# Kernel tuning notes

Hardware: AMD Instinct MI355X
Metric: run time of the kernel (lower is better)

## Reference

```python
import jax, jax.numpy as jnp
import numpy as np

B, S, D = 2, 2048, 1024
H, DK, DV = 16, 64, 64
MASKED = True


def setup_inputs() -> dict:
    key = jax.random.key(0)
    ks = jax.random.split(key, 12)
    s = 0.02
    inp = {
        "Q": jax.random.normal(ks[0], (B, S, D), jnp.float32),
        "K": jax.random.normal(ks[1], (B, S, D), jnp.float32),
        "V": jax.random.normal(ks[2], (B, S, D), jnp.float32),
        "pad_mask": jax.random.randint(ks[3], (B, S), 0, 2, jnp.int32),
        "Wq": jax.random.normal(ks[4], (D, H * DK), jnp.float32) * s,
        "bq": jnp.zeros((H * DK,), jnp.float32),
        "Wk": jax.random.normal(ks[5], (D, H * DK), jnp.float32) * s,
        "bk": jnp.zeros((H * DK,), jnp.float32),
        "Wv": jax.random.normal(ks[6], (D, H * DV), jnp.float32) * s,
        "bv": jnp.zeros((H * DV,), jnp.float32),
        "Wo": jax.random.normal(ks[7], (H * DV, D), jnp.float32) * s,
        "bo": jnp.zeros((D,), jnp.float32),
    }
    return inp


def _split(x):
    # [B,S,H*d] -> [B,H,S,d]
    b, s, _ = x.shape
    return x.reshape(b, s, H, -1).transpose(0, 2, 1, 3)


def reference(Q, K, V, pad_mask, Wq, bq, Wk, bk, Wv, bv, Wo, bo):
    q = _split(Q @ Wq + bq)  # [B,H,S,DK]
    k = _split(K @ Wk + bk)  # [B,H,S,DK]
    v = _split(V @ Wv + bv)  # [B,H,S,DV]

    scores = jnp.einsum("bhqd,bhkd->bhqk", q, k) / np.sqrt(DK)
    mask = pad_mask[:, None, None, :].astype(jnp.float32)  # [B,1,1,S]
    if MASKED:
        causal = jnp.triu(jnp.ones((S, S), jnp.float32), k=1)[None, None]
        mask = ((mask + causal) > 0).astype(jnp.float32)
    scores = scores - 1e9 * mask

    attn = jax.nn.softmax(scores, axis=-1)
    out = jnp.einsum("bhqk,bhkd->bhqd", attn, v)  # [B,H,S,DV]
    out = out.transpose(0, 2, 1, 3).reshape(B, S, H * DV)
    return out @ Wo + bo
```

## Files before the change

### kernel.cpp

```cpp
#include <hip/hip_runtime.h>

typedef unsigned short u16;
typedef unsigned int u32;

typedef __attribute__((ext_vector_type(8))) short bfrag;
typedef __attribute__((ext_vector_type(4))) float f32x4;
typedef __attribute__((ext_vector_type(8))) u16 u16x8;
typedef __attribute__((ext_vector_type(4))) u16 u16x4;

constexpr int S = 2048;
constexpr int HN = 16;
constexpr float QSCALE = 0.18033688011112042f;
constexpr float NBIG   = -1.442695e9f;

__device__ __forceinline__ u16 f2b(float f) {
  u32 u = __builtin_bit_cast(u32, f);
  return (u16)((u + 0x7FFFu + ((u >> 16) & 1u)) >> 16);
}
__device__ __forceinline__ float b2f(u16 v) {
  u32 u = (u32)v << 16;
  return __builtin_bit_cast(float, u);
}
__device__ __forceinline__ u32 cvtpk(float lo, float hi) {
  u32 d;
  asm("v_cvt_pk_bf16_f32 %0, %1, %2" : "=v"(d) : "v"(lo), "v"(hi));
  return d;
}
__device__ __forceinline__ float fexp2(float x) { return __builtin_amdgcn_exp2f(x); }

__device__ __forceinline__ f32x4 mfma16(bfrag a, bfrag b, f32x4 c) {
  return __builtin_amdgcn_mfma_f32_16x16x32_bf16(a, b, c, 0, 0, 0);
}

__device__ __forceinline__ void gload_lds16(const void* g, void* l) {
  __builtin_amdgcn_global_load_lds(
      (const __attribute__((address_space(1))) u32*)g,
      (__attribute__((address_space(3))) u32*)l, 16, 0, 0);
}

__global__ __launch_bounds__(256) void wtrans_kernel(
    const float* __restrict__ W0, const float* __restrict__ W1,
    const float* __restrict__ W2, const float* __restrict__ W3,
    u16* __restrict__ ws)
{
  const float* W = blockIdx.z == 0 ? W0 : blockIdx.z == 1 ? W1 : blockIdx.z == 2 ? W2 : W3;
  const float sc = blockIdx.z == 0 ? QSCALE : 1.0f;
  u16* WT = ws + (size_t)blockIdx.z * (1u << 20);
  __shared__ u16 tile[64 * 65];
  const int t = threadIdx.x;
  const int k0 = blockIdx.y * 64, n0 = blockIdx.x * 64;
#pragma unroll
  for (int i = 0; i < 4; ++i) {
    int idx = i * 256 + t;
    int r = idx >> 4, c4 = (idx & 15) * 4;
    float4 v = *(const float4*)&W[(size_t)(k0 + r) * 1024 + n0 + c4];
    tile[r * 65 + c4 + 0] = f2b(v.x * sc);
    tile[r * 65 + c4 + 1] = f2b(v.y * sc);
    tile[r * 65 + c4 + 2] = f2b(v.z * sc);
    tile[r * 65 + c4 + 3] = f2b(v.w * sc);
  }
  __syncthreads();
#pragma unroll
  for (int i = 0; i < 2; ++i) {
    int idx = i * 256 + t;
    int n = idx >> 3, k8 = (idx & 7) * 8;
    u16x8 o;
#pragma unroll
    for (int j = 0; j < 8; ++j) o[j] = tile[(k8 + j) * 65 + n];
    *(u16x8*)&WT[(size_t)(n0 + n) * 1024 + k0 + k8] = o;
  }
}

__global__ __launch_bounds__(256) void cvt_kernel(
    const float* __restrict__ A0, const float* __restrict__ A1,
    const float* __restrict__ A2, u16* __restrict__ outbase)
{
  const float* A = blockIdx.y == 0 ? A0 : blockIdx.y == 1 ? A1 : A2;
  u16* dst = outbase + (size_t)blockIdx.y * (4u << 20);
  size_t i = ((size_t)blockIdx.x * 256 + threadIdx.x) * 8;
  float4 v0 = *(const float4*)&A[i];
  float4 v1 = *(const float4*)&A[i + 4];
  union { u32 w[4]; u16x8 v; } o;
  o.w[0] = cvtpk(v0.x, v0.y); o.w[1] = cvtpk(v0.z, v0.w);
  o.w[2] = cvtpk(v1.x, v1.y); o.w[3] = cvtpk(v1.z, v1.w);
  *(u16x8*)&dst[i] = o.v;
}

__global__ __launch_bounds__(256) void pscan_kernel(
    const int* __restrict__ pad, u16* __restrict__ idxc, u16* __restrict__ posT,
    int* __restrict__ eqt, float* __restrict__ colsumg)
{
  __shared__ int wtot[4];
  __shared__ int cntS;
  const int b = blockIdx.x;
  const int t = threadIdx.x, lane = t & 63, w = t >> 6;
  for (int i = t; i < 1024; i += 256) colsumg[b * 1024 + i] = 0.f;
  int4 p0 = *(const int4*)&pad[b * 2048 + t * 8];
  int4 p1 = *(const int4*)&pad[b * 2048 + t * 8 + 4];
  int u[8] = {p0.x == 0, p0.y == 0, p0.z == 0, p0.w == 0,
              p1.x == 0, p1.y == 0, p1.z == 0, p1.w == 0};
  int ps[8], run = 0;
#pragma unroll
  for (int j = 0; j < 8; ++j) { run += u[j]; ps[j] = run; }
  int sc = run;
#pragma unroll
  for (int o = 1; o < 64; o <<= 1) {
    int v = __shfl_up(sc, o);
    if (lane >= o) sc += v;
  }
  if (lane == 63) wtot[w] = sc;
  __syncthreads();
  int base = 0;
#pragma unroll
  for (int i = 0; i < 4; ++i) if (i < w) base += wtot[i];
  int excl = base + sc - run;
#pragma unroll
  for (int j = 0; j < 8; ++j)
    if (u[j]) idxc[b * 2048 + excl + ps[j] - 1] = (u16)(t * 8 + j);
  if ((t & 7) == 7) eqt[b * 32 + (t >> 3)] = base + sc;
  if (t == 255) cntS = base + sc;
  __syncthreads();
  const int cnt = cntS;
#pragma unroll
  for (int j = 0; j < 8; ++j) {
    int e = t * 8 + j;
    int pv = u[j] ? (excl + ps[j] - 1) : (cnt + e - excl - ps[j]);
    posT[b * 2048 + e] = (u16)pv;
  }
  for (int j = cnt + t; j < 2048; j += 256) idxc[b * 2048 + j] = 0x7FFF;
}

__global__ __launch_bounds__(256) void vgather_kernel(
    const u16* __restrict__ vb, const u16* __restrict__ idxc, u16* __restrict__ vTc)
{
  __shared__ u16 tile[64 * 65];
  const int ti = blockIdx.x, bh = blockIdx.y, b = bh >> 4;
  const int t = threadIdx.x;
#pragma unroll
  for (int i = 0; i < 2; ++i) {
    int idx = i * 256 + t;
    int r = idx >> 3, c8 = (idx & 7) * 8;
    int o = idxc[b * 2048 + ti * 64 + r];
    u16x8 in = {};
    if (o != 0x7FFF) in = *(const u16x8*)&vb[((size_t)bh * 2048 + o) * 64 + c8];
#pragma unroll
    for (int j = 0; j < 8; ++j) tile[r * 65 + c8 + j] = in[j];
  }
  __syncthreads();
#pragma unroll
  for (int i = 0; i < 2; ++i) {
    int idx = i * 256 + t;
    int dv = idx >> 3, s8 = (idx & 7) * 8;
    u16x8 o_;
#pragma unroll
    for (int j = 0; j < 8; ++j) o_[j] = tile[(s8 + j) * 65 + dv];
    int a = s8 >> 5, bb = (s8 >> 4) & 1, cc = (s8 >> 3) & 1;
    int s0l = a * 32 + cc * 16 + bb * 4;
    int x = (dv & 7) << 3;
    u16x4 lo = {o_[0], o_[1], o_[2], o_[3]};
    u16x4 hi = {o_[4], o_[5], o_[6], o_[7]};
    size_t rowbase = ((size_t)bh * 64 + dv) * S + ti * 64;
    *(u16x4*)&vTc[rowbase + (s0l ^ x)] = lo;
    *(u16x4*)&vTc[rowbase + ((s0l + 8) ^ x)] = hi;
  }
}

template <int CMODE>
__device__ __forceinline__ void gemm_core(
    u16* As, u16* Bs,
    const u16* __restrict__ A, const u16* __restrict__ Bt,
    const float* __restrict__ bias, void* __restrict__ Cout,
    int N, int K, int bn, int bm, float bscale,
    const u16* __restrict__ posT, float* __restrict__ csum)
{
  const int tid = threadIdx.x;
  const int wid = tid >> 6, lane = tid & 63;
  const int g = lane >> 4, c = lane & 15;
  const int wr = wid >> 1, wc = wid & 1;

  f32x4 acc[4][2] = {};

  const int nkt = K >> 6;
  for (int kt = 0; kt < nkt; ++kt) {
#pragma unroll
    for (int p = 0; p < 4; ++p) {
      int off = (p * 4 + wid) * 1024 + (lane << 4);
      int row = off >> 7, colb = off & 127;
      gload_lds16(&A[(size_t)(bm * 128 + row) * K + kt * 64 +
                     ((colb ^ ((row & 7) << 4)) >> 1)],
                  (char*)As + (p * 4 + wid) * 1024);
    }
#pragma unroll
    for (int p = 0; p < 2; ++p) {
      int off = (p * 4 + wid) * 1024 + (lane << 4);
      int row = off >> 7, colb = off & 127;
      gload_lds16(&Bt[(size_t)(bn * 64 + row) * K + kt * 64 +
                      ((colb ^ ((row & 7) << 4)) >> 1)],
                  (char*)Bs + (p * 4 + wid) * 1024);
    }
    __syncthreads();

#pragma unroll
    for (int ks = 0; ks < 2; ++ks) {
      bfrag af[4], bf[2];
#pragma unroll
      for (int mi = 0; mi < 4; ++mi) {
        int row = wr * 64 + mi * 16 + c;
        af[mi] = *(const bfrag*)&As[row * 64 + ((ks * 32 + g * 8) ^ ((row & 7) << 3))];
      }
#pragma unroll
      for (int ni = 0; ni < 2; ++ni) {
        int row = wc * 32 + ni * 16 + c;
        bf[ni] = *(const bfrag*)&Bs[row * 64 + ((ks * 32 + g * 8) ^ ((row & 7) << 3))];
      }
#pragma unroll
      for (int mi = 0; mi < 4; ++mi)
#pragma unroll
        for (int ni = 0; ni < 2; ++ni)
          acc[mi][ni] = mfma16(af[mi], bf[ni], acc[mi][ni]);
    }
    __syncthreads();
  }

  float colacc[2] = {0.f, 0.f};
#pragma unroll
  for (int mi = 0; mi < 4; ++mi) {
#pragma unroll
    for (int ni = 0; ni < 2; ++ni) {
#pragma unroll
      for (int j = 0; j < 4; ++j) {
        int rowg = bm * 128 + wr * 64 + mi * 16 + g * 4 + j;
        int colg = bn * 64 + wc * 32 + ni * 16 + c;
        float val = fmaf(bias[colg], bscale, acc[mi][ni][j]);
        if (CMODE == 0) {
          int b = rowg >> 11, s = rowg & (S - 1);
          int h = colg >> 6, d = colg & 63;
          if (posT) {
            int p_ = posT[(b << 11) | s];
            s = p_;
            d = (d & 7) | ((((d >> 3) ^ p_) & 7) << 3);
          }
          if (csum) colacc[ni] += val;
          ((u16*)Cout)[((size_t)((b * HN + h) * S + s)) * 64 + d] = f2b(val);
        } else {
          ((float*)Cout)[(size_t)rowg * N + colg] = val;
        }
      }
    }
  }
  if (CMODE == 0 && csum) {
#pragma unroll
    for (int ni = 0; ni < 2; ++ni) {
      float s_ = colacc[ni];
      s_ += __shfl_xor(s_, 16);
      s_ += __shfl_xor(s_, 32);
      if (lane < 16) {
        int colg = bn * 64 + wc * 32 + ni * 16 + c;
        int b = (bm * 128) >> 11;
        atomicAdd(&csum[b * 1024 + colg], s_);
      }
    }
  }
}

__global__ __launch_bounds__(256) void qkv_gemm(
    const u16* __restrict__ Abase, const u16* __restrict__ WTbase,
    const float* __restrict__ b0, const float* __restrict__ b1, const float* __restrict__ b2,
    u16* __restrict__ qb, u16* __restrict__ kc, u16* __restrict__ vb,
    const u16* __restrict__ posT, float* __restrict__ colsumg)
{
  __shared__ __align__(16) u16 As[128 * 64];
  __shared__ __align__(16) u16 Bs[64 * 64];
  const int bid = blockIdx.x;
  const int l = (bid & 7) * 192 + (bid >> 3);
  const int z = l >> 9, rem = l & 511, bm = rem >> 4, bn = rem & 15;
  const u16* A = Abase + (size_t)z * (4u << 20);
  const u16* Bt = WTbase + (size_t)z * (1u << 20);
  const float* bias = z == 0 ? b0 : z == 1 ? b1 : b2;
  u16* C = z == 0 ? qb : z == 1 ? kc : vb;
  gemm_core<0>(As, Bs, A, Bt, bias, C, 1024, 1024, bn, bm,
               z == 0 ? QSCALE : 1.0f,
               z == 1 ? posT : nullptr,
               z == 2 ? colsumg : nullptr);
}

__global__ __launch_bounds__(256) void out_gemm(
    const u16* __restrict__ Av, const u16* __restrict__ Bt,
    const float* __restrict__ bias, void* __restrict__ Cout)
{
  __shared__ __align__(16) u16 As[128 * 64];
  __shared__ __align__(16) u16 Bs[64 * 64];
  const int bid = blockIdx.x;
  const int l = (bid & 7) * 64 + (bid >> 3);
  const int bm = l >> 4, bn = l & 15;
  gemm_core<1>(As, Bs, Av, Bt, bias, Cout, 1024, 1024, bn, bm, 1.0f,
               nullptr, nullptr);
}

__global__ __launch_bounds__(256) void attn_kernel(
    const u16* __restrict__ q, const u16* __restrict__ kc,
    const u16* __restrict__ vTc, const u16* __restrict__ idxc,
    const int* __restrict__ eqt, const float* __restrict__ colsumg,
    u16* __restrict__ ao)
{
  __shared__ __align__(16) u16 Ks[2][64 * 64];
  __shared__ __align__(16) u16 Vs[2][64 * 64];

  const int tid = threadIdx.x;
  const int wid = tid >> 6, lane = tid & 63;
  const int g = lane >> 4, c = lane & 15;
  const int i = blockIdx.x;
  const int qt = 31 - (i >> 5);
  const int bh = i & 31;
  const int b = bh >> 4, h = bh & 15;

  const u16* idxb = idxc + b * 2048;
  const int ecnt = eqt[b * 32 + qt];
  const int nt = (ecnt + 63) >> 6;
  const int fz = idxb[0];
  const int qbasew = qt * 64 + wid * 16;
  const int qrow = qbasew + c;

  bfrag qf[2];
#pragma unroll
  for (int ks = 0; ks < 2; ++ks)
    qf[ks] = *(const bfrag*)&q[((size_t)bh * S + qrow) * 64 + ks * 32 + g * 8];

  float m = -3.0e38f, lsum = 0.f;
  f32x4 acc[4] = {};

  const size_t kbase = (size_t)bh * S * 64;
  const size_t vbase = (size_t)bh * 64 * S;
  const int sb = wid * 2048 + (lane << 4);
  const int sb2 = sb + 1024;

#define STAGE(buf, t)                                                              \
  do {                                                                             \
    gload_lds16(&kc[kbase + (size_t)(t) * 4096 + (sb >> 1)],                       \
                (char*)Ks[buf] + wid * 2048);                                      \
    gload_lds16(&kc[kbase + (size_t)(t) * 4096 + (sb2 >> 1)],                      \
                (char*)Ks[buf] + wid * 2048 + 1024);                               \
    gload_lds16(&vTc[vbase + (size_t)(sb >> 7) * S + (t) * 64 + ((sb & 127) >> 1)],\
                (char*)Vs[buf] + wid * 2048);                                      \
    gload_lds16(&vTc[vbase + (size_t)(sb2 >> 7) * S + (t) * 64 + ((sb2 & 127) >> 1)],\
                (char*)Vs[buf] + wid * 2048 + 1024);                               \
  } while (0)

  if (nt > 0) {
    STAGE(0, 0);
    __syncthreads();

    int cur = 0;
    for (int t = 0; t < nt; ++t) {
      if (t + 1 < nt) { STAGE(cur ^ 1, t + 1); }

      f32x4 sc[4] = {};
      __builtin_amdgcn_s_setprio(1);
#pragma unroll
      for (int ks = 0; ks < 2; ++ks)
#pragma unroll
        for (int nf = 0; nf < 4; ++nf) {
          int row = nf * 16 + c;
          bfrag kf = *(const bfrag*)&Ks[cur][row * 64 + ((ks * 32 + g * 8) ^ ((row & 7) << 3))];
          sc[nf] = mfma16(kf, qf[ks], sc[nf]);
        }
      __builtin_amdgcn_s_setprio(0);

      float sval[4][4];
#pragma unroll
      for (int nf = 0; nf < 4; ++nf)
#pragma unroll
        for (int r = 0; r < 4; ++r) sval[nf][r] = sc[nf][r];

      if ((int)idxb[t * 64 + 63] > qbasew) {
#pragma unroll
        for (int nf = 0; nf < 4; ++nf)
#pragma unroll
          for (int r = 0; r < 4; ++r) {
            int ov = idxb[t * 64 + nf * 16 + g * 4 + r];
            if (ov > qrow) sval[nf][r] = NBIG;
          }
      }

      float pm = sval[0][0];
#pragma unroll
      for (int nf = 0; nf < 4; ++nf)
#pragma unroll
        for (int r = 0; r < 4; ++r) pm = fmaxf(pm, sval[nf][r]);
      pm = fmaxf(pm, __shfl_xor(pm, 16));
      pm = fmaxf(pm, __shfl_xor(pm, 32));
      if (!__all(pm - m <= 11.5416f)) {
        float mn = fmaxf(m, pm);
        float fac = fexp2(m - mn);
        lsum *= fac;
#pragma unroll
        for (int nf = 0; nf < 4; ++nf)
#pragma unroll
          for (int j = 0; j < 4; ++j) acc[nf][j] *= fac;
        m = mn;
      }
      float p16v[4][4];
      float rs = 0.f;
#pragma unroll
      for (int nf = 0; nf < 4; ++nf)
#pragma unroll
        for (int r = 0; r < 4; ++r) {
          float pv = fexp2(sval[nf][r] - m);
          p16v[nf][r] = pv;
          rs += pv;
        }
      rs += __shfl_xor(rs, 16);
      rs += __shfl_xor(rs, 32);
      lsum += rs;

      bfrag pa[2];
#pragma unroll
      for (int ks = 0; ks < 2; ++ks) {
        union { u32 w[4]; bfrag f; } pu;
#pragma unroll
        for (int tt = 0; tt < 4; ++tt)
          pu.w[tt] = cvtpk(p16v[2 * ks + (tt >> 1)][2 * (tt & 1)],
                           p16v[2 * ks + (tt >> 1)][2 * (tt & 1) + 1]);
        pa[ks] = pu.f;
      }

      __builtin_amdgcn_s_setprio(1);
#pragma unroll
      for (int ks = 0; ks < 2; ++ks)
#pragma unroll
        for (int nf = 0; nf < 4; ++nf) {
          int row = nf * 16 + c;
          bfrag vf = *(const bfrag*)&Vs[cur][row * 64 + ((ks * 32 + g * 8) ^ ((row & 7) << 3))];
          acc[nf] = mfma16(vf, pa[ks], acc[nf]);
        }
      __builtin_amdgcn_s_setprio(0);

      __syncthreads();
      cur ^= 1;
    }
  }
#undef STAGE

  const float inv = 1.f / lsum;
#pragma unroll
  for (int nf = 0; nf < 4; ++nf) {
    u16x4 ov;
    if (qrow < fz) {
#pragma unroll
      for (int j = 0; j < 4; ++j)
        ov[j] = f2b(colsumg[bh * 64 + nf * 16 + g * 4 + j] * (1.f / 2048.f));
    } else {
#pragma unroll
      for (int j = 0; j < 4; ++j) ov[j] = f2b(acc[nf][j] * inv);
    }
    *(u16x4*)&ao[((size_t)b * S + qrow) * 1024 + h * 64 + nf * 16 + g * 4] = ov;
  }
}

extern "C" void kernel_launch(void* const* d_in, const int* in_sizes, int n_in,
                              void* d_out, int out_size, void* d_ws, size_t ws_size,
                              hipStream_t stream)
{
  const float* Q  = (const float*)d_in[0];
  const float* Kk = (const float*)d_in[1];
  const float* V  = (const float*)d_in[2];
  const int* pad  = (const int*)d_in[3];
  const float* Wq = (const float*)d_in[4];
  const float* bq = (const float*)d_in[5];
  const float* Wk = (const float*)d_in[6];
  const float* bk = (const float*)d_in[7];
  const float* Wv = (const float*)d_in[8];
  const float* bv = (const float*)d_in[9];
  const float* Wo = (const float*)d_in[10];
  const float* bo = (const float*)d_in[11];

  u16* ws  = (u16*)d_ws;
  u16* WoT = ws + 3 * (size_t)(1u << 20);
  u16* qb  = ws + 4 * (size_t)(1u << 20);
  u16* kc  = ws + 8 * (size_t)(1u << 20);
  u16* vb  = ws + 12 * (size_t)(1u << 20);
  u16* vTc = ws + 16 * (size_t)(1u << 20);
  u16* Abf = ws + 20 * (size_t)(1u << 20);
  u16* tab = ws + 32 * (size_t)(1u << 20);
  float* colsumg = (float*)tab;
  u16* idxc = tab + 4096;
  u16* posT = tab + 8192;
  int* eqt  = (int*)(tab + 12288);
  u16* ao   = vb;

  wtrans_kernel<<<dim3(16, 16, 4), 256, 0, stream>>>(Wq, Wk, Wv, Wo, ws);
  pscan_kernel<<<2, 256, 0, stream>>>(pad, idxc, posT, eqt, colsumg);
  cvt_kernel<<<dim3(2048, 3), 256, 0, stream>>>(Q, Kk, V, Abf);
  qkv_gemm<<<1536, 256, 0, stream>>>(Abf, ws, bq, bk, bv, qb, kc, vb, posT, colsumg);
  vgather_kernel<<<dim3(32, 32), 256, 0, stream>>>(vb, idxc, vTc);
  attn_kernel<<<1024, 256, 0, stream>>>(qb, kc, vTc, idxc, eqt, colsumg, ao);
  out_gemm<<<512, 256, 0, stream>>>(ao, WoT, bo, d_out);
}
```

Before: 113.0 us.

## Double-buffer LDS tiles in GEMM core to overlap loads with MFMA

Splits the A/B shared-memory tiles into two buffers and prefetches the next K-tile into the alternate buffer while the current tile is consumed by MFMAs, cutting one barrier per iteration. The goal is to hide global-to-LDS load latency in the QKV and output projection GEMMs. It doubles LDS use per block to 48KB, which may lower occupancy. Correctness depends on the async direct-to-LDS loads having completed before the trailing barrier.

```diff
diff --git a/kernel.cpp b/kernel.cpp
--- a/kernel.cpp
+++ b/kernel.cpp
@@ -179,39 +179,47 @@
   const int wr = wid >> 1, wc = wid & 1;
 
   f32x4 acc[4][2] = {};
-
   const int nkt = K >> 6;
+
+#define GSTAGE(buf, kt)                                                         \
+  do {                                                                          \
+    _Pragma("unroll")                                                           \
+    for (int p = 0; p < 4; ++p) {                                               \
+      int off = (p * 4 + wid) * 1024 + (lane << 4);                             \
+      int row = off >> 7, colb = off & 127;                                     \
+      gload_lds16(&A[(size_t)(bm * 128 + row) * K + (kt) * 64 +                 \
+                     ((colb ^ ((row & 7) << 4)) >> 1)],                         \
+                  (char*)As + (buf) * 16384 + (p * 4 + wid) * 1024);            \
+    }                                                                           \
+    _Pragma("unroll")                                                           \
+    for (int p = 0; p < 2; ++p) {                                               \
+      int off = (p * 4 + wid) * 1024 + (lane << 4);                             \
+      int row = off >> 7, colb = off & 127;                                     \
+      gload_lds16(&Bt[(size_t)(bn * 64 + row) * K + (kt) * 64 +                 \
+                      ((colb ^ ((row & 7) << 4)) >> 1)],                        \
+                  (char*)Bs + (buf) * 8192 + (p * 4 + wid) * 1024);             \
+    }                                                                           \
+  } while (0)
+
+  GSTAGE(0, 0);
+  __syncthreads();
+  int cur = 0;
   for (int kt = 0; kt < nkt; ++kt) {
-#pragma unroll
-    for (int p = 0; p < 4; ++p) {
-      int off = (p * 4 + wid) * 1024 + (lane << 4);
-      int row = off >> 7, colb = off & 127;
-      gload_lds16(&A[(size_t)(bm * 128 + row) * K + kt * 64 +
-                     ((colb ^ ((row & 7) << 4)) >> 1)],
-                  (char*)As + (p * 4 + wid) * 1024);
-    }
-#pragma unroll
-    for (int p = 0; p < 2; ++p) {
-      int off = (p * 4 + wid) * 1024 + (lane << 4);
-      int row = off >> 7, colb = off & 127;
-      gload_lds16(&Bt[(size_t)(bn * 64 + row) * K + kt * 64 +
-                      ((colb ^ ((row & 7) << 4)) >> 1)],
-                  (char*)Bs + (p * 4 + wid) * 1024);
-    }
-    __syncthreads();
-
+    if (kt + 1 < nkt) GSTAGE(cur ^ 1, kt + 1);
 #pragma unroll
     for (int ks = 0; ks < 2; ++ks) {
       bfrag af[4], bf[2];
 #pragma unroll
       for (int mi = 0; mi < 4; ++mi) {
         int row = wr * 64 + mi * 16 + c;
-        af[mi] = *(const bfrag*)&As[row * 64 + ((ks * 32 + g * 8) ^ ((row & 7) << 3))];
+        af[mi] = *(const bfrag*)&As[cur * 8192 + row * 64 +
+                                    ((ks * 32 + g * 8) ^ ((row & 7) << 3))];
       }
 #pragma unroll
       for (int ni = 0; ni < 2; ++ni) {
         int row = wc * 32 + ni * 16 + c;
-        bf[ni] = *(const bfrag*)&Bs[row * 64 + ((ks * 32 + g * 8) ^ ((row & 7) << 3))];
+        bf[ni] = *(const bfrag*)&Bs[cur * 4096 + row * 64 +
+                                    ((ks * 32 + g * 8) ^ ((row & 7) << 3))];
       }
 #pragma unroll
       for (int mi = 0; mi < 4; ++mi)
@@ -220,7 +228,9 @@
           acc[mi][ni] = mfma16(af[mi], bf[ni], acc[mi][ni]);
     }
     __syncthreads();
-  }
+    cur ^= 1;
+  }
+#undef GSTAGE
 
   float colacc[2] = {0.f, 0.f};
 #pragma unroll
@@ -269,8 +279,8 @@
     u16* __restrict__ qb, u16* __restrict__ kc, u16* __restrict__ vb,
     const u16* __restrict__ posT, float* __restrict__ colsumg)
 {
-  __shared__ __align__(16) u16 As[128 * 64];
-  __shared__ __align__(16) u16 Bs[64 * 64];
+  __shared__ __align__(16) u16 As[2 * 128 * 64];
+  __shared__ __align__(16) u16 Bs[2 * 64 * 64];
   const int bid = blockIdx.x;
   const int l = (bid & 7) * 192 + (bid >> 3);
   const int z = l >> 9, rem = l & 511, bm = rem >> 4, bn = rem & 15;
@@ -288,8 +298,8 @@
     const u16* __restrict__ Av, const u16* __restrict__ Bt,
     const float* __restrict__ bias, void* __restrict__ Cout)
 {
-  __shared__ __align__(16) u16 As[128 * 64];
-  __shared__ __align__(16) u16 Bs[64 * 64];
+  __shared__ __align__(16) u16 As[2 * 128 * 64];
+  __shared__ __align__(16) u16 Bs[2 * 64 * 64];
   const int bid = blockIdx.x;
   const int l = (bid & 7) * 64 + (bid >> 3);
   const int bm = l >> 4, bn = l & 15;
```

Result: slower. 116.9 us (+3.5%).

## Compact K rows before projection and skip GEMM tiles for padded keys

Applied to the files above, without the earlier changes.

The K input rows are permuted into compacted (unpadded-first) order during the bf16 conversion using posT. The K projection GEMM can then skip whole 128-row tiles that lie beyond the count of valid keys, and the epilogue only applies a simple XOR swizzle instead of the posT-based scatter. This removes projection work for masked keys, which is roughly half of them for the random pad mask. It adds a posT lookup to the convert kernel and leaves a leftover no-op branch, and it relies on the attention kernel never reading kc rows past the valid count.

```diff
diff --git a/kernel.cpp b/kernel.cpp
--- a/kernel.cpp
+++ b/kernel.cpp
@@ -69,21 +69,6 @@
     for (int j = 0; j < 8; ++j) o[j] = tile[(k8 + j) * 65 + n];
     *(u16x8*)&WT[(size_t)(n0 + n) * 1024 + k0 + k8] = o;
   }
-}
-
-__global__ __launch_bounds__(256) void cvt_kernel(
-    const float* __restrict__ A0, const float* __restrict__ A1,
-    const float* __restrict__ A2, u16* __restrict__ outbase)
-{
-  const float* A = blockIdx.y == 0 ? A0 : blockIdx.y == 1 ? A1 : A2;
-  u16* dst = outbase + (size_t)blockIdx.y * (4u << 20);
-  size_t i = ((size_t)blockIdx.x * 256 + threadIdx.x) * 8;
-  float4 v0 = *(const float4*)&A[i];
-  float4 v1 = *(const float4*)&A[i + 4];
-  union { u32 w[4]; u16x8 v; } o;
-  o.w[0] = cvtpk(v0.x, v0.y); o.w[1] = cvtpk(v0.z, v0.w);
-  o.w[2] = cvtpk(v1.x, v1.y); o.w[3] = cvtpk(v1.z, v1.w);
-  *(u16x8*)&dst[i] = o.v;
 }
 
 __global__ __launch_bounds__(256) void pscan_kernel(
@@ -130,6 +115,33 @@
   for (int j = cnt + t; j < 2048; j += 256) idxc[b * 2048 + j] = 0x7FFF;
 }
 
+__global__ __launch_bounds__(256) void cvt_kernel(
+    const float* __restrict__ A0, const float* __restrict__ A1,
+    const float* __restrict__ A2, const u16* __restrict__ posT,
+    u16* __restrict__ outbase)
+{
+  const int z = blockIdx.y;
+  const float* A = z == 0 ? A0 : z == 1 ? A1 : A2;
+  u16* dst = outbase + (size_t)z * (4u << 20);
+  const int t = threadIdx.x;
+  const int row = blockIdx.x * 2 + (t >> 7);
+  const int col = (t & 127) * 8;
+  int drow = row;
+  if (z == 1) {
+    int b = row >> 11;
+    int p = posT[row];
+    if (p >= 2048 - ((b == 0) ? 0 : 0)) {  }
+    drow = b * 2048 + p;
+  }
+  const float* src = &A[(size_t)row * 1024 + col];
+  float4 v0 = *(const float4*)src;
+  float4 v1 = *(const float4*)(src + 4);
+  union { u32 w[4]; u16x8 v; } o;
+  o.w[0] = cvtpk(v0.x, v0.y); o.w[1] = cvtpk(v0.z, v0.w);
+  o.w[2] = cvtpk(v1.x, v1.y); o.w[3] = cvtpk(v1.z, v1.w);
+  *(u16x8*)&dst[(size_t)drow * 1024 + col] = o.v;
+}
+
 __global__ __launch_bounds__(256) void vgather_kernel(
     const u16* __restrict__ vb, const u16* __restrict__ idxc, u16* __restrict__ vTc)
 {
@@ -171,7 +183,7 @@
     const u16* __restrict__ A, const u16* __restrict__ Bt,
     const float* __restrict__ bias, void* __restrict__ Cout,
     int N, int K, int bn, int bm, float bscale,
-    const u16* __restrict__ posT, float* __restrict__ csum)
+    int kswz, float* __restrict__ csum)
 {
   const int tid = threadIdx.x;
   const int wid = tid >> 6, lane = tid & 63;
@@ -235,11 +247,7 @@
         if (CMODE == 0) {
           int b = rowg >> 11, s = rowg & (S - 1);
           int h = colg >> 6, d = colg & 63;
-          if (posT) {
-            int p_ = posT[(b << 11) | s];
-            s = p_;
-            d = (d & 7) | ((((d >> 3) ^ p_) & 7) << 3);
-          }
+          if (kswz) d ^= (s & 7) << 3;
           if (csum) colacc[ni] += val;
           ((u16*)Cout)[((size_t)((b * HN + h) * S + s)) * 64 + d] = f2b(val);
         } else {
@@ -267,20 +275,25 @@
     const u16* __restrict__ Abase, const u16* __restrict__ WTbase,
     const float* __restrict__ b0, const float* __restrict__ b1, const float* __restrict__ b2,
     u16* __restrict__ qb, u16* __restrict__ kc, u16* __restrict__ vb,
-    const u16* __restrict__ posT, float* __restrict__ colsumg)
+    const int* __restrict__ eqt, float* __restrict__ colsumg)
 {
   __shared__ __align__(16) u16 As[128 * 64];
   __shared__ __align__(16) u16 Bs[64 * 64];
   const int bid = blockIdx.x;
   const int l = (bid & 7) * 192 + (bid >> 3);
   const int z = l >> 9, rem = l & 511, bm = rem >> 4, bn = rem & 15;
+  if (z == 1) {
+    int b_ = (bm * 128) >> 11;
+    int cnt_ = eqt[b_ * 32 + 31];
+    if (((bm * 128) & 2047) >= cnt_) return;
+  }
   const u16* A = Abase + (size_t)z * (4u << 20);
   const u16* Bt = WTbase + (size_t)z * (1u << 20);
   const float* bias = z == 0 ? b0 : z == 1 ? b1 : b2;
   u16* C = z == 0 ? qb : z == 1 ? kc : vb;
   gemm_core<0>(As, Bs, A, Bt, bias, C, 1024, 1024, bn, bm,
                z == 0 ? QSCALE : 1.0f,
-               z == 1 ? posT : nullptr,
+               z == 1 ? 1 : 0,
                z == 2 ? colsumg : nullptr);
 }
 
@@ -294,7 +307,7 @@
   const int l = (bid & 7) * 64 + (bid >> 3);
   const int bm = l >> 4, bn = l & 15;
   gemm_core<1>(As, Bs, Av, Bt, bias, Cout, 1024, 1024, bn, bm, 1.0f,
-               nullptr, nullptr);
+               0, nullptr);
 }
 
 __global__ __launch_bounds__(256) void attn_kernel(
@@ -490,8 +503,8 @@
 
   wtrans_kernel<<<dim3(16, 16, 4), 256, 0, stream>>>(Wq, Wk, Wv, Wo, ws);
   pscan_kernel<<<2, 256, 0, stream>>>(pad, idxc, posT, eqt, colsumg);
-  cvt_kernel<<<dim3(2048, 3), 256, 0, stream>>>(Q, Kk, V, Abf);
-  qkv_gemm<<<1536, 256, 0, stream>>>(Abf, ws, bq, bk, bv, qb, kc, vb, posT, colsumg);
+  cvt_kernel<<<dim3(2048, 3), 256, 0, stream>>>(Q, Kk, V, posT, Abf);
+  qkv_gemm<<<1536, 256, 0, stream>>>(Abf, ws, bq, bk, bv, qb, kc, vb, eqt, colsumg);
   vgather_kernel<<<dim3(32, 32), 256, 0, stream>>>(vb, idxc, vTc);
   attn_kernel<<<1024, 256, 0, stream>>>(qb, kc, vTc, idxc, eqt, colsumg, ao);
   out_gemm<<<512, 256, 0, stream>>>(ao, WoT, bo, d_out);
```

New measurement: 105.3 us. -6.8%, faster.
